# Kernel optimization log

Measured on AMD Instinct MI355X. Metric: run time of the kernel, lower is better.

## Reference

```python
import jax, jax.numpy as jnp
import numpy as np

B, IN_CH, OUT_CH, N_MAPS, H, W_DIM, CTRL = 64, 32, 32, 64, 64, 64, 512
NF = N_MAPS                # forget gate units
NI = IN_CH * N_MAPS       # input gate units
NO = OUT_CH * N_MAPS      # output gate units


def setup_inputs() -> dict:
    key = jax.random.key(0)
    k1, k2, k3, k4 = jax.random.split(key, 4)
    inputs = jax.random.normal(k1, (B, IN_CH, H, W_DIM), dtype=jnp.float32)
    state = jax.random.normal(k2, (B, N_MAPS, H, W_DIM), dtype=jnp.float32)
    controls = jax.random.normal(k3, (B, CTRL), dtype=jnp.float32)
    Wc = jax.random.normal(k4, (NF + NI + NO, CTRL), dtype=jnp.float32) * (CTRL ** -0.5)
    return {"inputs": inputs, "state": state, "controls": controls, "W": Wc}


def reference(inputs, state, controls, W):
    # control linear (no bias): [B, NF+NI+NO]
    ctrl = controls @ W.T
    f = ctrl[:, :NF]                         # [B, n_maps]
    i = ctrl[:, NF:NF + NI]                  # [B, in_ch*n_maps]
    o = ctrl[:, NF + NI:]                    # [B, out_ch*n_maps]
    in_gates = i.reshape(B, N_MAPS, IN_CH)   # per-sample 1x1 conv filters
    forget_gates = f.reshape(B, N_MAPS, 1, 1)
    out_gates = o.reshape(B, OUT_CH, N_MAPS)
    # per-sample 1x1 conv == batched channel contraction
    gated_inputs = jnp.einsum('bchw,bmc->bmhw', inputs, in_gates)
    new_state = gated_inputs + state * forget_gates
    output = jnp.tanh(new_state)
    outputs = jnp.einsum('bmhw,bom->bohw', output, out_gates)
    return (outputs, new_state)
```

## Files before the change

kernel.cpp:

```cpp
#include <hip/hip_runtime.h>
#include <cstdint>
#include <cstddef>

#define B_SZ   64
#define IN_CH  32
#define OUT_CH 32
#define NMAPS  64
#define HW     4096
#define CTRLN  512
#define NROWS  4160
#define OUT0_SZ (B_SZ*OUT_CH*HW)
#define TILE   128

typedef short bf8_t  __attribute__((ext_vector_type(8)));
typedef short bf4_t  __attribute__((ext_vector_type(4)));
typedef float f32x4  __attribute__((ext_vector_type(4)));

__device__ __forceinline__ unsigned short f2bf(float f) {
    union { float f; uint32_t u; } v; v.f = f;
    return (unsigned short)((v.u + 0x7FFFu + ((v.u >> 16) & 1u)) >> 16);
}
__device__ __forceinline__ float fast_tanh(float x) {
    float e = __expf(2.0f * x);
    return 1.0f - 2.0f * __builtin_amdgcn_rcpf(e + 1.0f);
}

__global__ __launch_bounds__(256) void ctrl_gemm(
    const float* __restrict__ controls, const float* __restrict__ W,
    float* __restrict__ ws)
{
    __shared__ __align__(16) float ct[128 * 65];
    const int tid = threadIdx.x;
    const int b   = tid & 63;
    const int w   = __builtin_amdgcn_readfirstlane(tid >> 6);
    const int j0  = blockIdx.x * 8 + w * 2;
    const float* w0 = W + (size_t)j0 * CTRLN;

    float acc0 = 0.f, acc1 = 0.f;
    for (int kc = 0; kc < CTRLN; kc += 128) {
        __syncthreads();
#pragma unroll
        for (int i = 0; i < 8; ++i) {
            const int flat = (i * 256 + tid) * 4;
            const int bb = flat >> 7;
            const int kk = flat & 127;
            float4 v = *(const float4*)(controls + (size_t)bb * CTRLN + kc + kk);
            ct[(kk + 0) * 65 + bb] = v.x;
            ct[(kk + 1) * 65 + bb] = v.y;
            ct[(kk + 2) * 65 + bb] = v.z;
            ct[(kk + 3) * 65 + bb] = v.w;
        }
        __syncthreads();
#pragma unroll 8
        for (int k = 0; k < 128; ++k) {
            const float c = ct[k * 65 + b];
            acc0 += w0[kc + k] * c;
            acc1 += w0[CTRLN + kc + k] * c;
        }
    }
    ws[(size_t)b * NROWS + j0]     = acc0;
    ws[(size_t)b * NROWS + j0 + 1] = acc1;
}

__global__ __launch_bounds__(256, 4) void vstm_main(
    const float* __restrict__ inputs, const float* __restrict__ state,
    const float* __restrict__ ws, float* __restrict__ out)
{
    __shared__ __align__(16) unsigned short Xt[TILE * 40];
    __shared__ __align__(16) unsigned short IGs[64 * 40];
    __shared__ __align__(16) unsigned short OGs[32 * 72];
    __shared__ __align__(16) unsigned short Tt[TILE * 72];
    __shared__ __align__(16) float fs[64];

    const int tid  = threadIdx.x;
    const int b    = blockIdx.y;
    const int tile = blockIdx.x * TILE;
    const int w    = __builtin_amdgcn_readfirstlane(tid >> 6);
    const int l    = tid & 63;
    const int quad = l >> 4;
    const int mlo  = l & 15;

    const float* g = ws + (size_t)b * NROWS;
    if (tid < 64) fs[tid] = g[tid];
#pragma unroll
    for (int i = 0; i < 2; ++i) {
        const int e = (i * 256 + tid) * 4;
        float4 gi = *(const float4*)(g + 64 + e);
        bf4_t vi = { (short)f2bf(gi.x), (short)f2bf(gi.y),
                     (short)f2bf(gi.z), (short)f2bf(gi.w) };
        *(bf4_t*)&IGs[(e >> 5) * 40 + (e & 31)] = vi;
        float4 go = *(const float4*)(g + 2112 + e);
        bf4_t vo = { (short)f2bf(go.x), (short)f2bf(go.y),
                     (short)f2bf(go.z), (short)f2bf(go.w) };
        *(bf4_t*)&OGs[(e >> 6) * 72 + (e & 63)] = vo;
    }
    const float* inb = inputs + (size_t)b * IN_CH * HW + tile;
#pragma unroll
    for (int i = 0; i < 16; ++i) {
        const int flat = i * 256 + tid;
        const int c = flat >> 7, p = flat & 127;
        Xt[p * 40 + c] = f2bf(inb[c * HW + p]);
    }
    __syncthreads();

    bf8_t af[2], bg[4];
#pragma unroll
    for (int pc = 0; pc < 2; ++pc)
        af[pc] = *(const bf8_t*)&Xt[(w * 32 + pc * 16 + mlo) * 40 + quad * 8];
#pragma unroll
    for (int mc = 0; mc < 4; ++mc)
        bg[mc] = *(const bf8_t*)&IGs[(mc * 16 + mlo) * 40 + quad * 8];

    f32x4 acc[2][4];
#pragma unroll
    for (int pc = 0; pc < 2; ++pc)
#pragma unroll
        for (int mc = 0; mc < 4; ++mc) {
            acc[pc][mc] = (f32x4){0.f, 0.f, 0.f, 0.f};
            acc[pc][mc] = __builtin_amdgcn_mfma_f32_16x16x32_bf16(
                af[pc], bg[mc], acc[pc][mc], 0, 0, 0);
        }

    const float* stb = state + (size_t)b * NMAPS * HW + tile;
    float*       nsb = out + OUT0_SZ + (size_t)b * NMAPS * HW + tile;
#pragma unroll
    for (int mc = 0; mc < 4; ++mc) {
        const int m = mc * 16 + mlo;
        const float fgt = fs[m];
#pragma unroll
        for (int pc = 0; pc < 2; ++pc) {
            const int p0 = w * 32 + pc * 16 + quad * 4;
            const float4 st = *(const float4*)(stb + (size_t)m * HW + p0);
            float4 ns;
            ns.x = acc[pc][mc][0] + st.x * fgt;
            ns.y = acc[pc][mc][1] + st.y * fgt;
            ns.z = acc[pc][mc][2] + st.z * fgt;
            ns.w = acc[pc][mc][3] + st.w * fgt;
            *(float4*)(nsb + (size_t)m * HW + p0) = ns;
            Tt[(p0 + 0) * 72 + m] = f2bf(fast_tanh(ns.x));
            Tt[(p0 + 1) * 72 + m] = f2bf(fast_tanh(ns.y));
            Tt[(p0 + 2) * 72 + m] = f2bf(fast_tanh(ns.z));
            Tt[(p0 + 3) * 72 + m] = f2bf(fast_tanh(ns.w));
        }
    }

    bf8_t ag[2][2], at[2][2];
#pragma unroll
    for (int oc = 0; oc < 2; ++oc)
#pragma unroll
        for (int ks = 0; ks < 2; ++ks)
            ag[oc][ks] = *(const bf8_t*)&OGs[(oc * 16 + mlo) * 72 + ks * 32 + quad * 8];
#pragma unroll
    for (int pc = 0; pc < 2; ++pc)
#pragma unroll
        for (int ks = 0; ks < 2; ++ks)
            at[pc][ks] = *(const bf8_t*)&Tt[(w * 32 + pc * 16 + mlo) * 72 + ks * 32 + quad * 8];

    f32x4 acc2[2][2];
#pragma unroll
    for (int pc = 0; pc < 2; ++pc)
#pragma unroll
        for (int oc = 0; oc < 2; ++oc) {
            acc2[pc][oc] = (f32x4){0.f, 0.f, 0.f, 0.f};
#pragma unroll
            for (int ks = 0; ks < 2; ++ks)
                acc2[pc][oc] = __builtin_amdgcn_mfma_f32_16x16x32_bf16(
                    at[pc][ks], ag[oc][ks], acc2[pc][oc], 0, 0, 0);
        }

    float* ob = out + (size_t)b * OUT_CH * HW + tile;
#pragma unroll
    for (int pc = 0; pc < 2; ++pc)
#pragma unroll
        for (int oc = 0; oc < 2; ++oc) {
            const int p0 = w * 32 + pc * 16 + quad * 4;
            const int o  = oc * 16 + mlo;
            float4 r;
            r.x = acc2[pc][oc][0];
            r.y = acc2[pc][oc][1];
            r.z = acc2[pc][oc][2];
            r.w = acc2[pc][oc][3];
            *(float4*)(ob + (size_t)o * HW + p0) = r;
        }
}

extern "C" void kernel_launch(void* const* d_in, const int* in_sizes, int n_in,
                              void* d_out, int out_size, void* d_ws, size_t ws_size,
                              hipStream_t stream) {
    const float* inputs   = (const float*)d_in[0];
    const float* state    = (const float*)d_in[1];
    const float* controls = (const float*)d_in[2];
    const float* W        = (const float*)d_in[3];
    float*       out      = (float*)d_out;
    float*       ws       = (float*)d_ws;

    ctrl_gemm<<<dim3(NROWS / 8), 256, 0, stream>>>(controls, W, ws);

    dim3 g2(HW / TILE, B_SZ);
    vstm_main<<<g2, 256, 0, stream>>>(inputs, state, ws, out);
}
```

Baseline: 223.3 us.

## Use split-bf16 MFMA for control GEMM and prefetch inputs/state into registers

Rewrites the control linear layer to run on MFMA with a three-term bf16 hi/lo split that approximates fp32 accuracy, replacing the scalar FMA loop that staged controls through shared memory. The main kernel now loads its input fragments directly from global memory into registers, dropping the Xt transpose tile, and issues the state loads early so they overlap the gate setup. Shared memory is aliased between IGs and Tt, with an extra barrier added, which allows launch bounds of 5 blocks per unit. The split-bf16 GEMM carries a small precision risk, and the uncoalesced strided input loads could cost bandwidth.

```diff
diff --git a/kernel.cpp b/kernel.cpp
--- a/kernel.cpp
+++ b/kernel.cpp
@@ -20,6 +20,10 @@
     union { float f; uint32_t u; } v; v.f = f;
     return (unsigned short)((v.u + 0x7FFFu + ((v.u >> 16) & 1u)) >> 16);
 }
+__device__ __forceinline__ float bf2f(unsigned short h) {
+    union { uint32_t u; float f; } v; v.u = (uint32_t)h << 16;
+    return v.f;
+}
 __device__ __forceinline__ float fast_tanh(float x) {
     float e = __expf(2.0f * x);
     return 1.0f - 2.0f * __builtin_amdgcn_rcpf(e + 1.0f);
@@ -29,48 +33,56 @@
     const float* __restrict__ controls, const float* __restrict__ W,
     float* __restrict__ ws)
 {
-    __shared__ __align__(16) float ct[128 * 65];
-    const int tid = threadIdx.x;
-    const int b   = tid & 63;
-    const int w   = __builtin_amdgcn_readfirstlane(tid >> 6);
-    const int j0  = blockIdx.x * 8 + w * 2;
-    const float* w0 = W + (size_t)j0 * CTRLN;
-
-    float acc0 = 0.f, acc1 = 0.f;
-    for (int kc = 0; kc < CTRLN; kc += 128) {
-        __syncthreads();
-#pragma unroll
-        for (int i = 0; i < 8; ++i) {
-            const int flat = (i * 256 + tid) * 4;
-            const int bb = flat >> 7;
-            const int kk = flat & 127;
-            float4 v = *(const float4*)(controls + (size_t)bb * CTRLN + kc + kk);
-            ct[(kk + 0) * 65 + bb] = v.x;
-            ct[(kk + 1) * 65 + bb] = v.y;
-            ct[(kk + 2) * 65 + bb] = v.z;
-            ct[(kk + 3) * 65 + bb] = v.w;
-        }
-        __syncthreads();
-#pragma unroll 8
-        for (int k = 0; k < 128; ++k) {
-            const float c = ct[k * 65 + b];
-            acc0 += w0[kc + k] * c;
-            acc1 += w0[CTRLN + kc + k] * c;
-        }
-    }
-    ws[(size_t)b * NROWS + j0]     = acc0;
-    ws[(size_t)b * NROWS + j0 + 1] = acc1;
-}
-
-__global__ __launch_bounds__(256, 4) void vstm_main(
+    const int tid  = threadIdx.x;
+    const int l    = tid & 63;
+    const int w    = __builtin_amdgcn_readfirstlane(tid >> 6);
+    const int quad = l >> 4;
+    const int mlo  = l & 15;
+    const int j0   = blockIdx.x * 16;
+
+    const float* wr = W + (size_t)(j0 + mlo) * CTRLN;
+    const float* cr = controls + (size_t)(w * 16 + mlo) * CTRLN;
+
+    f32x4 acc = {0.f, 0.f, 0.f, 0.f};
+#pragma unroll 4
+    for (int ks = 0; ks < 16; ++ks) {
+        const int k0 = ks * 32 + quad * 8;
+        const float4 a0 = *(const float4*)(wr + k0);
+        const float4 a1 = *(const float4*)(wr + k0 + 4);
+        const float4 b0 = *(const float4*)(cr + k0);
+        const float4 b1 = *(const float4*)(cr + k0 + 4);
+        const float av[8] = {a0.x,a0.y,a0.z,a0.w,a1.x,a1.y,a1.z,a1.w};
+        const float bv[8] = {b0.x,b0.y,b0.z,b0.w,b1.x,b1.y,b1.z,b1.w};
+        bf8_t ah, al_, bh, bl;
+#pragma unroll
+        for (int e = 0; e < 8; ++e) {
+            const unsigned short hA = f2bf(av[e]);
+            ah[e]  = (short)hA;
+            al_[e] = (short)f2bf(av[e] - bf2f(hA));
+            const unsigned short hB = f2bf(bv[e]);
+            bh[e]  = (short)hB;
+            bl[e]  = (short)f2bf(bv[e] - bf2f(hB));
+        }
+        acc = __builtin_amdgcn_mfma_f32_16x16x32_bf16(ah,  bh, acc, 0, 0, 0);
+        acc = __builtin_amdgcn_mfma_f32_16x16x32_bf16(ah,  bl, acc, 0, 0, 0);
+        acc = __builtin_amdgcn_mfma_f32_16x16x32_bf16(al_, bh, acc, 0, 0, 0);
+    }
+
+    const int bidx = w * 16 + mlo;
+    float4 r;
+    r.x = acc[0]; r.y = acc[1]; r.z = acc[2]; r.w = acc[3];
+    *(float4*)(ws + (size_t)bidx * NROWS + j0 + quad * 4) = r;
+}
+
+__global__ __launch_bounds__(256, 5) void vstm_main(
     const float* __restrict__ inputs, const float* __restrict__ state,
     const float* __restrict__ ws, float* __restrict__ out)
 {
-    __shared__ __align__(16) unsigned short Xt[TILE * 40];
-    __shared__ __align__(16) unsigned short IGs[64 * 40];
-    __shared__ __align__(16) unsigned short OGs[32 * 72];
-    __shared__ __align__(16) unsigned short Tt[TILE * 72];
-    __shared__ __align__(16) float fs[64];
+    __shared__ __align__(16) unsigned char smem[23296];
+    unsigned short* const IGs = (unsigned short*)(smem);
+    unsigned short* const Tt  = (unsigned short*)(smem);
+    unsigned short* const OGs = (unsigned short*)(smem + 18432);
+    float*          const fs  = (float*)(smem + 23040);
 
     const int tid  = threadIdx.x;
     const int b    = blockIdx.y;
@@ -81,35 +93,58 @@
     const int mlo  = l & 15;
 
     const float* g = ws + (size_t)b * NROWS;
-    if (tid < 64) fs[tid] = g[tid];
+    const float fsv = g[tid & 63];
+    float4 giv[2], gov[2];
 #pragma unroll
     for (int i = 0; i < 2; ++i) {
         const int e = (i * 256 + tid) * 4;
-        float4 gi = *(const float4*)(g + 64 + e);
-        bf4_t vi = { (short)f2bf(gi.x), (short)f2bf(gi.y),
-                     (short)f2bf(gi.z), (short)f2bf(gi.w) };
+        giv[i] = *(const float4*)(g + 64 + e);
+        gov[i] = *(const float4*)(g + 2112 + e);
+    }
+
+    const float* xb = inputs + (size_t)b * IN_CH * HW + tile + w * 32;
+    float xf[2][8];
+#pragma unroll
+    for (int pc = 0; pc < 2; ++pc)
+#pragma unroll
+        for (int j = 0; j < 8; ++j)
+            xf[pc][j] = xb[(size_t)(quad * 8 + j) * HW + pc * 16 + mlo];
+
+    const float* stb = state + (size_t)b * NMAPS * HW + tile;
+    float4 stv[4][2];
+#pragma unroll
+    for (int mc = 0; mc < 4; ++mc)
+#pragma unroll
+        for (int pc = 0; pc < 2; ++pc)
+            stv[mc][pc] = *(const float4*)(stb + (size_t)(mc * 16 + mlo) * HW
+                                           + w * 32 + pc * 16 + quad * 4);
+
+    if (tid < 64) fs[tid] = fsv;
+#pragma unroll
+    for (int i = 0; i < 2; ++i) {
+        const int e = (i * 256 + tid) * 4;
+        bf4_t vi = { (short)f2bf(giv[i].x), (short)f2bf(giv[i].y),
+                     (short)f2bf(giv[i].z), (short)f2bf(giv[i].w) };
         *(bf4_t*)&IGs[(e >> 5) * 40 + (e & 31)] = vi;
-        float4 go = *(const float4*)(g + 2112 + e);
-        bf4_t vo = { (short)f2bf(go.x), (short)f2bf(go.y),
-                     (short)f2bf(go.z), (short)f2bf(go.w) };
+        bf4_t vo = { (short)f2bf(gov[i].x), (short)f2bf(gov[i].y),
+                     (short)f2bf(gov[i].z), (short)f2bf(gov[i].w) };
         *(bf4_t*)&OGs[(e >> 6) * 72 + (e & 63)] = vo;
     }
-    const float* inb = inputs + (size_t)b * IN_CH * HW + tile;
-#pragma unroll
-    for (int i = 0; i < 16; ++i) {
-        const int flat = i * 256 + tid;
-        const int c = flat >> 7, p = flat & 127;
-        Xt[p * 40 + c] = f2bf(inb[c * HW + p]);
-    }
     __syncthreads();
 
-    bf8_t af[2], bg[4];
-#pragma unroll
-    for (int pc = 0; pc < 2; ++pc)
-        af[pc] = *(const bf8_t*)&Xt[(w * 32 + pc * 16 + mlo) * 40 + quad * 8];
+    bf8_t bg[4];
 #pragma unroll
     for (int mc = 0; mc < 4; ++mc)
         bg[mc] = *(const bf8_t*)&IGs[(mc * 16 + mlo) * 40 + quad * 8];
+
+    bf8_t af[2];
+#pragma unroll
+    for (int pc = 0; pc < 2; ++pc)
+#pragma unroll
+        for (int j = 0; j < 8; ++j)
+            af[pc][j] = (short)f2bf(xf[pc][j]);
+
+    __syncthreads();
 
     f32x4 acc[2][4];
 #pragma unroll
@@ -121,8 +156,7 @@
                 af[pc], bg[mc], acc[pc][mc], 0, 0, 0);
         }
 
-    const float* stb = state + (size_t)b * NMAPS * HW + tile;
-    float*       nsb = out + OUT0_SZ + (size_t)b * NMAPS * HW + tile;
+    float* nsb = out + OUT0_SZ + (size_t)b * NMAPS * HW + tile;
 #pragma unroll
     for (int mc = 0; mc < 4; ++mc) {
         const int m = mc * 16 + mlo;
@@ -130,7 +164,7 @@
 #pragma unroll
         for (int pc = 0; pc < 2; ++pc) {
             const int p0 = w * 32 + pc * 16 + quad * 4;
-            const float4 st = *(const float4*)(stb + (size_t)m * HW + p0);
+            const float4 st = stv[mc][pc];
             float4 ns;
             ns.x = acc[pc][mc][0] + st.x * fgt;
             ns.y = acc[pc][mc][1] + st.y * fgt;
@@ -194,7 +228,7 @@
     float*       out      = (float*)d_out;
     float*       ws       = (float*)d_ws;
 
-    ctrl_gemm<<<dim3(NROWS / 8), 256, 0, stream>>>(controls, W, ws);
+    ctrl_gemm<<<dim3(NROWS / 16), 256, 0, stream>>>(controls, W, ws);
 
     dim3 g2(HW / TILE, B_SZ);
     vstm_main<<<g2, 256, 0, stream>>>(inputs, state, ws, out);
```

New measurement: 209.4 us. 1.07x faster.
